# Kernel tuning notes

Hardware: AMD Instinct MI355X
Metric: run time of the kernel (lower is better)

## Reference

```python
import jax, jax.numpy as jnp
import numpy as np

N = 100000
E = 6400000
H = 64  # hidden_nf


def setup_inputs() -> dict:
    key = jax.random.key(0)
    ks = jax.random.split(key, 12)
    x = jax.random.normal(ks[0], (N, 3), dtype=jnp.float32)
    vel = jax.random.normal(ks[1], (N, 3), dtype=jnp.float32)
    vel_norm = jax.random.uniform(ks[2], (N, 1), dtype=jnp.float32)
    edge_index = jax.random.randint(ks[3], (2, E), 0, N, dtype=jnp.int32)
    # coord_mlp_vel: Linear(1,H) -> LeakyReLU(0.2) -> Linear(H,1)
    W1 = jax.random.normal(ks[4], (H, 1), dtype=jnp.float32) * (1.0 / np.sqrt(1))
    b1 = jnp.zeros((H,), dtype=jnp.float32)
    W2 = jax.random.normal(ks[5], (1, H), dtype=jnp.float32) * (1.0 / np.sqrt(H))
    b2 = jnp.zeros((1,), dtype=jnp.float32)
    # phi: Linear(1,H) -> LeakyReLU(0.2) -> Linear(H,1,bias=False, xavier gain=0.001) -> Tanh
    Wp1 = jax.random.normal(ks[6], (H, 1), dtype=jnp.float32) * (1.0 / np.sqrt(1))
    bp1 = jnp.zeros((H,), dtype=jnp.float32)
    Wp2 = jax.random.normal(ks[7], (1, H), dtype=jnp.float32) * 0.001
    return {"x": x, "vel_norm": vel_norm, "vel": vel, "edge_index": edge_index,
            "W1": W1, "b1": b1, "W2": W2, "b2": b2,
            "Wp1": Wp1, "bp1": bp1, "Wp2": Wp2}


def reference(x, vel_norm, vel, edge_index, W1, b1, W2, b2, Wp1, bp1, Wp2):
    row, col = edge_index[0], edge_index[1]
    # edge_model: gather endpoint positions, radial distance -> tiny MLP -> scaled diff
    x_diff = x[row] - x[col]                                   # [E, 3]
    radial = jnp.sqrt(jnp.sum(x_diff * x_diff, axis=1, keepdims=True))  # [E, 1]
    h = jax.nn.leaky_relu(radial @ Wp1.T + bp1, 0.2)           # [E, H]
    e_out = jnp.tanh(h @ Wp2.T)                                # [E, 1]
    m_ij = x_diff * e_out                                      # [E, 3]
    # node_model: unsorted_segment_mean over row
    agg_sum = jax.ops.segment_sum(m_ij, row, num_segments=x.shape[0])           # [N, 3]
    cnt = jax.ops.segment_sum(jnp.ones((m_ij.shape[0], 1), m_ij.dtype), row,
                              num_segments=x.shape[0])                           # [N, 1]
    x_out = x + agg_sum / jnp.maximum(cnt, 1.0)
    # velocity term: x + vel * coord_mlp_vel(vel_norm)
    hv = jax.nn.leaky_relu(vel_norm @ W1.T + b1, 0.2)          # [N, H]
    scale = hv @ W2.T + b2                                     # [N, 1]
    return x_out + vel * scale
```

## Files before the change

### kernel.cpp

```cpp
#include <hip/hip_runtime.h>
#include <hip/hip_fp16.h>
#include <math.h>

#define LEAKY 0.2f
#define HDIM 64
#define EPB 2048
#define TPB1 256
#define PERT (EPB / TPB1)
#define RANGE 1024
#define RSH 10
#define KMAX 128
#define NSLICE 12
#define FIXS 4194304.0f
#define INVFIXS (1.0f / 4194304.0f)


__global__ void precompute_kernel(const float* __restrict__ Wp1,
                                  const float* __restrict__ bp1,
                                  const float* __restrict__ Wp2,
                                  float* __restrict__ consts) {
    int k = threadIdx.x;
    float w1 = Wp1[k];
    float slope = (w1 >= 0.f) ? 1.f : LEAKY;
    float c = Wp2[k] * w1 * slope;
    float bnz = (bp1[k] != 0.f) ? 1.f : 0.f;
    #pragma unroll
    for (int off = 32; off > 0; off >>= 1) {
        c += __shfl_down(c, off, 64);
        bnz += __shfl_down(bnz, off, 64);
    }
    if (k == 0) { consts[0] = c; consts[1] = bnz; }
}

__device__ __forceinline__ float fast_tanh(float v) {
    float e = __builtin_amdgcn_exp2f(v * 2.88539008178f);
    return 1.0f - 2.0f * __builtin_amdgcn_rcpf(e + 1.0f);
}

__device__ __forceinline__ float edge_eo(float rad, float C, bool slow,
                                         const float* sW1, const float* sb1,
                                         const float* sW2) {
    if (!slow) return fast_tanh(C * rad);
    float a = 0.f;
    #pragma unroll
    for (int k = 0; k < HDIM; k++) {
        float h = fmaf(rad, sW1[k], sb1[k]);
        h = (h > 0.f) ? h : LEAKY * h;
        a = fmaf(sW2[k], h, a);
    }
    return fast_tanh(a);
}

__global__ void repack_kernel(const float* __restrict__ x, float4* __restrict__ x4, int N) {
    int i = blockIdx.x * blockDim.x + threadIdx.x;
    if (i < N) x4[i] = make_float4(x[3*i], x[3*i+1], x[3*i+2], 0.f);
}

__global__ void repack_h_kernel(const float* __restrict__ x, uint2* __restrict__ xh, int N) {
    int i = blockIdx.x * blockDim.x + threadIdx.x;
    if (i < N) {
        unsigned hx = __half_as_ushort(__float2half(x[3*i]));
        unsigned hy = __half_as_ushort(__float2half(x[3*i+1]));
        unsigned hz = __half_as_ushort(__float2half(x[3*i+2]));
        xh[i] = make_uint2((hy << 16) | hx, hz);
    }
}

__device__ __forceinline__ unsigned long long pack_rec(float dx, float dy, float dz,
                                                       float eo, unsigned lid) {
    unsigned hx = __half_as_ushort(__float2half(dx * eo));
    unsigned hy = __half_as_ushort(__float2half(dy * eo));
    unsigned hz = __half_as_ushort(__float2half(dz * eo));
    return (unsigned long long)lid
         | ((unsigned long long)hx << 11)
         | ((unsigned long long)hy << 27)
         | ((unsigned long long)hz << 43);
}

__device__ __forceinline__ uint2 make_record(uint2 ga, uint2 gb, int r,
                                             float C, bool slow,
                                             const float* sW1, const float* sb1,
                                             const float* sW2) {
    float ax = __half2float(__ushort_as_half((unsigned short)(ga.x & 0xFFFF)));
    float ay = __half2float(__ushort_as_half((unsigned short)(ga.x >> 16)));
    float az = __half2float(__ushort_as_half((unsigned short)(ga.y & 0xFFFF)));
    float bx = __half2float(__ushort_as_half((unsigned short)(gb.x & 0xFFFF)));
    float by = __half2float(__ushort_as_half((unsigned short)(gb.x >> 16)));
    float bz = __half2float(__ushort_as_half((unsigned short)(gb.y & 0xFFFF)));
    float dx = ax - bx, dy = ay - by, dz = az - bz;
    float rad = sqrtf(dx*dx + dy*dy + dz*dz);
    float eo = edge_eo(rad, C, slow, sW1, sb1, sW2);
    unsigned long long u = pack_rec(dx, dy, dz, eo, (unsigned)r & (RANGE - 1));
    return make_uint2((unsigned)u, (unsigned)(u >> 32));
}

__global__ __launch_bounds__(TPB1) void compute_kernel(
        const uint2* __restrict__ xh,
        const int* __restrict__ ei,
        const float* __restrict__ Wp1, const float* __restrict__ bp1,
        const float* __restrict__ Wp2, const float* __restrict__ consts,
        uint2* __restrict__ rec_raw, unsigned* __restrict__ histG, int E, int K) {
    __shared__ unsigned hist[4][KMAX];
    __shared__ float sW1[HDIM], sb1[HDIM], sW2[HDIM];
    const float C = consts[0];
    const bool slow = (consts[1] != 0.f);
    if (slow) {
        for (int k = threadIdx.x; k < HDIM; k += TPB1) {
            sW1[k] = Wp1[k]; sb1[k] = bp1[k]; sW2[k] = Wp2[k];
        }
    }
    int w = threadIdx.x >> 6;
    for (int k = threadIdx.x; k < 4 * KMAX; k += TPB1) ((unsigned*)hist)[k] = 0;
    __syncthreads();

    const size_t base = (size_t)blockIdx.x * EPB;
    const unsigned t = threadIdx.x;
    if (base + EPB <= (size_t)E && (E & 3) == 0) {
        const int4* pr = (const int4*)(ei + base);
        const int4* pc = (const int4*)(ei + (size_t)E + base);
        int4* po = (int4*)(rec_raw + base);
        const int HALFI4 = EPB / 4;
        #pragma unroll
        for (int i = 0; i < PERT / 4; i++) {
            unsigned idx = t + i * TPB1;
            int4 rv = pr[idx];
            int4 cv = pc[idx];
            uint2 ga0 = xh[rv.x], gb0 = xh[cv.x];
            uint2 ga1 = xh[rv.y], gb1 = xh[cv.y];
            uint2 ga2 = xh[rv.z], gb2 = xh[cv.z];
            uint2 ga3 = xh[rv.w], gb3 = xh[cv.w];
            uint2 r0 = make_record(ga0, gb0, rv.x, C, slow, sW1, sb1, sW2);
            uint2 r1 = make_record(ga1, gb1, rv.y, C, slow, sW1, sb1, sW2);
            uint2 r2 = make_record(ga2, gb2, rv.z, C, slow, sW1, sb1, sW2);
            uint2 r3 = make_record(ga3, gb3, rv.w, C, slow, sW1, sb1, sW2);
            atomicAdd(&hist[w][((unsigned)rv.x) >> RSH], 1u);
            atomicAdd(&hist[w][((unsigned)rv.y) >> RSH], 1u);
            atomicAdd(&hist[w][((unsigned)rv.z) >> RSH], 1u);
            atomicAdd(&hist[w][((unsigned)rv.w) >> RSH], 1u);
            po[idx]          = make_int4((int)r0.x, (int)r0.y, (int)r1.x, (int)r1.y);
            po[HALFI4 + idx] = make_int4((int)r2.x, (int)r2.y, (int)r3.x, (int)r3.y);
        }
    } else {
        for (int i = 0; i < PERT; i++) {
            size_t e = base + (size_t)i * TPB1 + t;
            if (e < (size_t)E) {
                int r = ei[e];
                int c = ei[(size_t)E + e];
                uint2 ga = xh[r], gb = xh[c];
                uint2 rec = make_record(ga, gb, r, C, slow, sW1, sb1, sW2);
                rec_raw[e] = rec;
                atomicAdd(&hist[w][((unsigned)r) >> RSH], 1u);
            }
        }
    }
    __syncthreads();
    for (int k = threadIdx.x; k < K; k += TPB1)
        histG[(size_t)blockIdx.x * K + k] = hist[0][k] + hist[1][k] + hist[2][k] + hist[3][k];
}

__global__ __launch_bounds__(256) void colscan_kernel(unsigned* __restrict__ histG,
                                                      unsigned* __restrict__ totals,
                                                      int nblk, int K) {
    __shared__ unsigned pa[256], pb[256];
    const int b = blockIdx.x;
    const int t = threadIdx.x;
    const int chunk = (nblk + 255) / 256;
    const int r0 = t * chunk;
    unsigned s = 0;
    for (int i = 0; i < chunk; i++) {
        int r = r0 + i;
        if (r < nblk) s += histG[(size_t)r * K + b];
    }
    pa[t] = s;
    __syncthreads();
    unsigned* src = pa; unsigned* dst = pb;
    for (int off = 1; off < 256; off <<= 1) {
        unsigned v = src[t];
        if (t >= off) v += src[t - off];
        dst[t] = v;
        __syncthreads();
        unsigned* tmp = src; src = dst; dst = tmp;
    }
    unsigned excl = (t > 0) ? src[t - 1] : 0u;
    if (t == 255) totals[b] = src[255];
    unsigned run = excl;
    for (int i = 0; i < chunk; i++) {
        int r = r0 + i;
        if (r < nblk) {
            size_t a = (size_t)r * K + b;
            unsigned v = histG[a];
            histG[a] = run;
            run += v;
        }
    }
}

__global__ void base_scan_kernel(const unsigned* __restrict__ totals,
                                 unsigned* __restrict__ base, int K) {
    if (threadIdx.x == 0) {
        unsigned acc = 0;
        for (int k = 0; k < K; k++) { base[k] = acc; acc += totals[k]; }
        base[K] = acc;
    }
}

__global__ __launch_bounds__(TPB1) void sort_kernel(
        const int* __restrict__ ei, const uint2* __restrict__ rec_raw,
        const unsigned* __restrict__ histG, const unsigned* __restrict__ basep,
        uint2* __restrict__ recs, int E, int K) {
    __shared__ uint2 stage[EPB];
    __shared__ unsigned char bucket_of[EPB];
    __shared__ unsigned hist[KMAX];
    __shared__ unsigned scanv[KMAX + 1];
    __shared__ unsigned gstart[KMAX];
    for (int k = threadIdx.x; k < K; k += TPB1) hist[k] = 0;
    __syncthreads();

    const size_t base = (size_t)blockIdx.x * EPB;
    const bool perm = (base + EPB <= (size_t)E) && ((E & 3) == 0);
    uint2 rc[PERT];
    unsigned bk[PERT];
    #pragma unroll
    for (int i = 0; i < PERT; i++) {
        size_t e = base + (size_t)i * TPB1 + threadIdx.x;
        bk[i] = 0xFFFFFFFFu;
        if (e < (size_t)E) {
            size_t pos = e;
            if (perm) {
                unsigned j = (unsigned)(e - base);
                pos = base + ((size_t)((j >> 1) & 1u) * (EPB / 2))
                           + ((j >> 2) << 1) + (j & 1u);
            }
            rc[i] = rec_raw[pos];
            unsigned b_ = ((unsigned)ei[e]) >> RSH;
            bk[i] = b_;
            atomicAdd(&hist[b_], 1u);
        }
    }
    __syncthreads();
    if (threadIdx.x == 0) {
        unsigned a = 0;
        for (int k = 0; k < K; k++) { scanv[k] = a; a += hist[k]; }
        scanv[K] = a;
    }
    __syncthreads();
    if (threadIdx.x < (unsigned)K)
        gstart[threadIdx.x] = basep[threadIdx.x]
                            + histG[(size_t)blockIdx.x * K + threadIdx.x];
    for (int k = threadIdx.x; k < K; k += TPB1) hist[k] = scanv[k];
    __syncthreads();
    #pragma unroll
    for (int i = 0; i < PERT; i++) {
        if (bk[i] != 0xFFFFFFFFu) {
            unsigned slot = atomicAdd(&hist[bk[i]], 1u);
            stage[slot] = rc[i];
            bucket_of[slot] = (unsigned char)bk[i];
        }
    }
    __syncthreads();
    unsigned total = scanv[K];
    for (unsigned j = threadIdx.x; j < total; j += TPB1) {
        unsigned b_ = bucket_of[j];
        recs[(size_t)gstart[b_] + (j - scanv[b_])] = stage[j];
    }
}

__global__ __launch_bounds__(TPB1) void count_kernel(const int* __restrict__ ei,
                                                     unsigned* __restrict__ cnts,
                                                     int E, int K) {
    __shared__ unsigned hist[4][KMAX];
    int w = threadIdx.x >> 6;
    for (int k = threadIdx.x; k < 4 * KMAX; k += TPB1) ((unsigned*)hist)[k] = 0;
    __syncthreads();
    int base = blockIdx.x * EPB;
    #pragma unroll
    for (int i = 0; i < PERT; i++) {
        int e = base + i * TPB1 + threadIdx.x;
        if (e < E) atomicAdd(&hist[w][((unsigned)ei[e]) >> RSH], 1u);
    }
    __syncthreads();
    for (int k = threadIdx.x; k < K; k += TPB1) {
        unsigned t = hist[0][k] + hist[1][k] + hist[2][k] + hist[3][k];
        if (t) atomicAdd(&cnts[k], t);
    }
}

__global__ void scan_kernel(const unsigned* __restrict__ cnts,
                            unsigned* __restrict__ base,
                            unsigned* __restrict__ cursor, int K) {
    if (threadIdx.x == 0) {
        unsigned acc = 0;
        for (int k = 0; k < K; k++) { base[k] = acc; cursor[k] = acc; acc += cnts[k]; }
        base[K] = acc;
    }
}

__global__ __launch_bounds__(TPB1) void bin_kernel(
        const float* __restrict__ x, const float4* __restrict__ x4, int use4,
        const int* __restrict__ ei,
        const float* __restrict__ Wp1, const float* __restrict__ bp1,
        const float* __restrict__ Wp2, const float* __restrict__ consts,
        unsigned* __restrict__ cursor, uint2* __restrict__ recs, int E, int K) {
    __shared__ uint2 stage[EPB];
    __shared__ unsigned char bucket_of[EPB];
    __shared__ unsigned hist[KMAX];
    __shared__ unsigned scanv[KMAX + 1];
    __shared__ unsigned gstart[KMAX];
    __shared__ float sW1[HDIM], sb1[HDIM], sW2[HDIM];
    const float C = consts[0];
    const bool slow = (consts[1] != 0.f);
    if (slow) {
        for (int k = threadIdx.x; k < HDIM; k += TPB1) {
            sW1[k] = Wp1[k]; sb1[k] = bp1[k]; sW2[k] = Wp2[k];
        }
    }
    for (int k = threadIdx.x; k < K; k += TPB1) hist[k] = 0;
    __syncthreads();

    int base = blockIdx.x * EPB;
    uint2 rc[PERT];
    unsigned bk[PERT];
    #pragma unroll
    for (int i = 0; i < PERT; i++) {
        int e = base + i * TPB1 + threadIdx.x;
        bk[i] = 0xFFFFFFFFu;
        if (e < E) {
            int r = ei[e];
            int c = ei[(size_t)E + e];
            float dx, dy, dz;
            if (use4) {
                float4 a = x4[r], b = x4[c];
                dx = a.x - b.x; dy = a.y - b.y; dz = a.z - b.z;
            } else {
                dx = x[3*r]   - x[3*c];
                dy = x[3*r+1] - x[3*c+1];
                dz = x[3*r+2] - x[3*c+2];
            }
            float rad = sqrtf(dx*dx + dy*dy + dz*dz);
            float eo = edge_eo(rad, C, slow, sW1, sb1, sW2);
            unsigned long long u = pack_rec(dx, dy, dz, eo, (unsigned)r & (RANGE - 1));
            rc[i] = make_uint2((unsigned)u, (unsigned)(u >> 32));
            bk[i] = (unsigned)r >> RSH;
            atomicAdd(&hist[bk[i]], 1u);
        }
    }
    __syncthreads();
    if (threadIdx.x == 0) {
        unsigned a = 0;
        for (int k = 0; k < K; k++) { scanv[k] = a; a += hist[k]; }
        scanv[K] = a;
    }
    __syncthreads();
    if (threadIdx.x < (unsigned)K) {
        unsigned c_ = scanv[threadIdx.x + 1] - scanv[threadIdx.x];
        gstart[threadIdx.x] = c_ ? atomicAdd(&cursor[threadIdx.x], c_) : 0u;
    }
    for (int k = threadIdx.x; k < K; k += TPB1) hist[k] = scanv[k];
    __syncthreads();
    #pragma unroll
    for (int i = 0; i < PERT; i++) {
        if (bk[i] != 0xFFFFFFFFu) {
            unsigned slot = atomicAdd(&hist[bk[i]], 1u);
            stage[slot] = rc[i];
            bucket_of[slot] = (unsigned char)bk[i];
        }
    }
    __syncthreads();
    unsigned total = scanv[K];
    for (unsigned j = threadIdx.x; j < total; j += TPB1) {
        unsigned b_ = bucket_of[j];
        recs[(size_t)gstart[b_] + (j - scanv[b_])] = stage[j];
    }
}

__device__ __forceinline__ void proc_rec(uint2 r, unsigned (*acc)[RANGE]) {
    unsigned long long u = ((unsigned long long)r.y << 32) | r.x;
    unsigned lid = (unsigned)(u & (RANGE - 1));
    float mx = __half2float(__ushort_as_half((unsigned short)((u >> 11) & 0xFFFF)));
    float my = __half2float(__ushort_as_half((unsigned short)((u >> 27) & 0xFFFF)));
    float mz = __half2float(__ushort_as_half((unsigned short)((u >> 43) & 0xFFFF)));
    atomicAdd(&acc[0][lid], (unsigned)(int)__float2int_rn(mx * FIXS));
    atomicAdd(&acc[1][lid], (unsigned)(int)__float2int_rn(my * FIXS));
    atomicAdd(&acc[2][lid], (unsigned)(int)__float2int_rn(mz * FIXS));
    atomicAdd(&acc[3][lid], 1u);
}

__global__ __launch_bounds__(256) void reduce_kernel(
        const uint2* __restrict__ recs, const unsigned* __restrict__ base,
        float4* __restrict__ slices, int N, int K) {
    __shared__ unsigned acc[4][RANGE];
    int b = blockIdx.x / NSLICE;
    int s = blockIdx.x % NSLICE;
    for (int i = threadIdx.x; i < RANGE; i += 256) {
        acc[0][i] = 0u; acc[1][i] = 0u; acc[2][i] = 0u; acc[3][i] = 0u;
    }
    __syncthreads();
    unsigned lo = base[b], hi = base[b + 1];
    unsigned cnt = hi - lo;
    unsigned per = (cnt + NSLICE - 1) / NSLICE;
    unsigned st = lo + (unsigned)s * per;
    unsigned en = st + per; if (en > hi) en = hi;
    unsigned j = st + threadIdx.x;
    if (st < hi) {
        while (j + 256 < en) {
            uint2 r0 = recs[j];
            uint2 r1 = recs[j + 256];
            proc_rec(r0, acc);
            proc_rec(r1, acc);
            j += 512;
        }
        while (j < en) { proc_rec(recs[j], acc); j += 256; }
    }
    __syncthreads();
    int nbase = b * RANGE;
    for (int i = threadIdx.x; i < RANGE; i += 256) {
        int node = nbase + i;
        if (node < N)
            slices[(size_t)s * N + node] =
                make_float4((float)(int)acc[0][i] * INVFIXS,
                            (float)(int)acc[1][i] * INVFIXS,
                            (float)(int)acc[2][i] * INVFIXS,
                            (float)acc[3][i]);
    }
}

__global__ void node_kernel(const float* __restrict__ x, const float* __restrict__ vel_norm,
                            const float* __restrict__ vel,
                            const float* __restrict__ W1, const float* __restrict__ b1,
                            const float* __restrict__ W2, const float* __restrict__ b2,
                            const float4* __restrict__ slices,
                            float* __restrict__ out, int N, int S) {
    __shared__ float sW1[HDIM], sb1[HDIM], sW2[HDIM];
    for (int k = threadIdx.x; k < HDIM; k += blockDim.x) {
        sW1[k] = W1[k]; sb1[k] = b1[k]; sW2[k] = W2[k];
    }
    __syncthreads();
    int i = blockIdx.x * blockDim.x + threadIdx.x;
    if (i >= N) return;
    float sx = 0.f, sy = 0.f, sz = 0.f, sc = 0.f;
    for (int s = 0; s < S; s++) {
        float4 v = slices[(size_t)s * N + i];
        sx += v.x; sy += v.y; sz += v.z; sc += v.w;
    }
    float vn = vel_norm[i];
    float a = b2[0];
    #pragma unroll
    for (int k = 0; k < HDIM; k++) {
        float h = fmaf(vn, sW1[k], sb1[k]);
        h = (h > 0.f) ? h : LEAKY * h;
        a = fmaf(sW2[k], h, a);
    }
    float inv = 1.0f / fmaxf(sc, 1.0f);
    out[3*i]     = x[3*i]     + sx * inv + vel[3*i]     * a;
    out[3*i + 1] = x[3*i + 1] + sy * inv + vel[3*i + 1] * a;
    out[3*i + 2] = x[3*i + 2] + sz * inv + vel[3*i + 2] * a;
}

__global__ void edge_atomic_kernel(const float* __restrict__ x, const int* __restrict__ ei,
                                   const float* __restrict__ Wp1, const float* __restrict__ bp1,
                                   const float* __restrict__ Wp2, const float* __restrict__ consts,
                                   float* __restrict__ acc, int E) {
    __shared__ float sW1[HDIM], sb1[HDIM], sW2[HDIM];
    const float C = consts[0];
    const bool slow = (consts[1] != 0.f);
    if (slow) {
        for (int k = threadIdx.x; k < HDIM; k += blockDim.x) {
            sW1[k] = Wp1[k]; sb1[k] = bp1[k]; sW2[k] = Wp2[k];
        }
        __syncthreads();
    }
    int e = blockIdx.x * blockDim.x + threadIdx.x;
    if (e >= E) return;
    int r = ei[e];
    int c = ei[E + e];
    float dx = x[3*r] - x[3*c];
    float dy = x[3*r+1] - x[3*c+1];
    float dz = x[3*r+2] - x[3*c+2];
    float rad = sqrtf(dx*dx + dy*dy + dz*dz);
    float eo = edge_eo(rad, C, slow, sW1, sb1, sW2);
    float* basep = acc + ((size_t)r << 2);
    atomicAdd(basep + 0, dx * eo);
    atomicAdd(basep + 1, dy * eo);
    atomicAdd(basep + 2, dz * eo);
    atomicAdd(basep + 3, 1.f);
}

extern "C" void kernel_launch(void* const* d_in, const int* in_sizes, int n_in,
                              void* d_out, int out_size, void* d_ws, size_t ws_size,
                              hipStream_t stream) {
    const float* x        = (const float*)d_in[0];
    const float* vel_norm = (const float*)d_in[1];
    const float* vel      = (const float*)d_in[2];
    const int*   ei       = (const int*)  d_in[3];
    const float* W1       = (const float*)d_in[4];
    const float* b1       = (const float*)d_in[5];
    const float* W2       = (const float*)d_in[6];
    const float* b2       = (const float*)d_in[7];
    const float* Wp1      = (const float*)d_in[8];
    const float* bp1      = (const float*)d_in[9];
    const float* Wp2      = (const float*)d_in[10];

    const int N = in_sizes[0] / 3;
    const int E = in_sizes[3] / 2;
    const int K = (N + RANGE - 1) / RANGE;
    const int nblk = (E + EPB - 1) / EPB;

    size_t rec_bytes   = (size_t)E * sizeof(uint2);
    size_t slice_bytes = (size_t)NSLICE * N * sizeof(float4);
    size_t x4_bytes    = (size_t)N * sizeof(float4);
    size_t histG_bytes = (size_t)nblk * K * sizeof(unsigned);

    size_t sp_raw   = rec_bytes;
    size_t sp_x4    = sp_raw + (rec_bytes > slice_bytes ? rec_bytes : slice_bytes);
    size_t sp_hist  = sp_x4 + x4_bytes;
    size_t sp_tot   = sp_hist + histG_bytes;
    size_t sp_base  = sp_tot + (size_t)K * sizeof(unsigned);
    size_t sp_const = (sp_base + (size_t)(K + 1) * sizeof(unsigned) + 15) & ~(size_t)15;
    size_t need_split = sp_const + 32;

    size_t small_bytes = (size_t)(KMAX + (KMAX + 1) + KMAX) * sizeof(unsigned) + 32;
    size_t fu_recs  = slice_bytes;
    size_t fu_x4    = fu_recs + rec_bytes;
    size_t fu_small = fu_x4 + x4_bytes;
    size_t need_fused = fu_small + small_bytes;

    if (K <= KMAX && ws_size >= need_split) {
        uint2*    recs   = (uint2*)   d_ws;
        uint2*    raw    = (uint2*)   ((char*)d_ws + sp_raw);
        float4*   slices = (float4*)  ((char*)d_ws + sp_raw);
        uint2*    xh     = (uint2*)   ((char*)d_ws + sp_x4);
        unsigned* histG  = (unsigned*)((char*)d_ws + sp_hist);
        unsigned* totals = (unsigned*)((char*)d_ws + sp_tot);
        unsigned* basep  = (unsigned*)((char*)d_ws + sp_base);
        float*    consts = (float*)   ((char*)d_ws + sp_const);

        precompute_kernel<<<1, 64, 0, stream>>>(Wp1, bp1, Wp2, consts);
        repack_h_kernel<<<(N + 255) / 256, 256, 0, stream>>>(x, xh, N);
        compute_kernel<<<nblk, TPB1, 0, stream>>>(xh, ei, Wp1, bp1, Wp2, consts,
                                                  raw, histG, E, K);
        colscan_kernel<<<K, 256, 0, stream>>>(histG, totals, nblk, K);
        base_scan_kernel<<<1, 64, 0, stream>>>(totals, basep, K);
        sort_kernel<<<nblk, TPB1, 0, stream>>>(ei, raw, histG, basep, recs, E, K);
        reduce_kernel<<<K * NSLICE, 256, 0, stream>>>(recs, basep, slices, N, K);
        node_kernel<<<(N + 255) / 256, 256, 0, stream>>>(x, vel_norm, vel, W1, b1, W2, b2,
                                                         slices, (float*)d_out, N, NSLICE);
    } else if (K <= KMAX && ws_size >= need_fused) {
        float4*   slices = (float4*)  d_ws;
        uint2*    recs   = (uint2*)   ((char*)d_ws + fu_recs);
        float4*   x4     = (float4*)  ((char*)d_ws + fu_x4);
        unsigned* cnts   = (unsigned*)((char*)d_ws + fu_small);
        unsigned* basep  = cnts + KMAX;
        unsigned* cursor = basep + KMAX + 1;
        float*    consts = (float*)(cursor + KMAX);

        hipMemsetAsync(cnts, 0, small_bytes, stream);
        precompute_kernel<<<1, 64, 0, stream>>>(Wp1, bp1, Wp2, consts);
        repack_kernel<<<(N + 255) / 256, 256, 0, stream>>>(x, x4, N);
        count_kernel<<<nblk, TPB1, 0, stream>>>(ei, cnts, E, K);
        scan_kernel<<<1, 64, 0, stream>>>(cnts, basep, cursor, K);
        bin_kernel<<<nblk, TPB1, 0, stream>>>(x, x4, 1, ei, Wp1, bp1, Wp2, consts,
                                              cursor, recs, E, K);
        reduce_kernel<<<K * NSLICE, 256, 0, stream>>>(recs, basep, slices, N, K);
        node_kernel<<<(N + 255) / 256, 256, 0, stream>>>(x, vel_norm, vel, W1, b1, W2, b2,
                                                         slices, (float*)d_out, N, NSLICE);
    } else {
        float* acc    = (float*)d_ws;
        float* consts = (float*)((char*)d_ws + (size_t)N * sizeof(float4));
        hipMemsetAsync(d_ws, 0, (size_t)N * sizeof(float4) + 32, stream);
        precompute_kernel<<<1, 64, 0, stream>>>(Wp1, bp1, Wp2, consts);
        edge_atomic_kernel<<<(E + 255) / 256, 256, 0, stream>>>(x, ei, Wp1, bp1, Wp2,
                                                                consts, acc, E);
        node_kernel<<<(N + 255) / 256, 256, 0, stream>>>(x, vel_norm, vel, W1, b1, W2, b2,
                                                         (const float4*)acc, (float*)d_out, N, 1);
    }
}
```

Measured before the change: 223.6 us.

## Fuse edge record computation into sort pass, replace compute with count-only histogram

The first pass now only reads row indices to build per-block bucket histograms, and the sort pass itself gathers endpoint positions, computes the edge records and scatters them. This removes the write and re-read of the intermediate raw record array (8 bytes per edge each way). The cost is that the count pass reads the row indices separately and the sort kernel carries more register pressure from the gather and MLP work. The workspace layout drops the raw buffer aliasing.

```diff
diff --git a/kernel.cpp b/kernel.cpp
--- a/kernel.cpp
+++ b/kernel.cpp
@@ -94,64 +94,27 @@
     return make_uint2((unsigned)u, (unsigned)(u >> 32));
 }
 
-__global__ __launch_bounds__(TPB1) void compute_kernel(
-        const uint2* __restrict__ xh,
-        const int* __restrict__ ei,
-        const float* __restrict__ Wp1, const float* __restrict__ bp1,
-        const float* __restrict__ Wp2, const float* __restrict__ consts,
-        uint2* __restrict__ rec_raw, unsigned* __restrict__ histG, int E, int K) {
+__global__ __launch_bounds__(TPB1) void count2_kernel(const int* __restrict__ ei,
+                                                      unsigned* __restrict__ histG,
+                                                      int E, int K) {
     __shared__ unsigned hist[4][KMAX];
-    __shared__ float sW1[HDIM], sb1[HDIM], sW2[HDIM];
-    const float C = consts[0];
-    const bool slow = (consts[1] != 0.f);
-    if (slow) {
-        for (int k = threadIdx.x; k < HDIM; k += TPB1) {
-            sW1[k] = Wp1[k]; sb1[k] = bp1[k]; sW2[k] = Wp2[k];
-        }
-    }
     int w = threadIdx.x >> 6;
     for (int k = threadIdx.x; k < 4 * KMAX; k += TPB1) ((unsigned*)hist)[k] = 0;
     __syncthreads();
-
     const size_t base = (size_t)blockIdx.x * EPB;
-    const unsigned t = threadIdx.x;
-    if (base + EPB <= (size_t)E && (E & 3) == 0) {
-        const int4* pr = (const int4*)(ei + base);
-        const int4* pc = (const int4*)(ei + (size_t)E + base);
-        int4* po = (int4*)(rec_raw + base);
-        const int HALFI4 = EPB / 4;
+    if (base + EPB <= (size_t)E) {
+        const int4* p = (const int4*)(ei + base);
         #pragma unroll
-        for (int i = 0; i < PERT / 4; i++) {
-            unsigned idx = t + i * TPB1;
-            int4 rv = pr[idx];
-            int4 cv = pc[idx];
-            uint2 ga0 = xh[rv.x], gb0 = xh[cv.x];
-            uint2 ga1 = xh[rv.y], gb1 = xh[cv.y];
-            uint2 ga2 = xh[rv.z], gb2 = xh[cv.z];
-            uint2 ga3 = xh[rv.w], gb3 = xh[cv.w];
-            uint2 r0 = make_record(ga0, gb0, rv.x, C, slow, sW1, sb1, sW2);
-            uint2 r1 = make_record(ga1, gb1, rv.y, C, slow, sW1, sb1, sW2);
-            uint2 r2 = make_record(ga2, gb2, rv.z, C, slow, sW1, sb1, sW2);
-            uint2 r3 = make_record(ga3, gb3, rv.w, C, slow, sW1, sb1, sW2);
-            atomicAdd(&hist[w][((unsigned)rv.x) >> RSH], 1u);
-            atomicAdd(&hist[w][((unsigned)rv.y) >> RSH], 1u);
-            atomicAdd(&hist[w][((unsigned)rv.z) >> RSH], 1u);
-            atomicAdd(&hist[w][((unsigned)rv.w) >> RSH], 1u);
-            po[idx]          = make_int4((int)r0.x, (int)r0.y, (int)r1.x, (int)r1.y);
-            po[HALFI4 + idx] = make_int4((int)r2.x, (int)r2.y, (int)r3.x, (int)r3.y);
+        for (int i = 0; i < EPB / 4 / TPB1; i++) {
+            int4 v = p[threadIdx.x + i * TPB1];
+            atomicAdd(&hist[w][((unsigned)v.x) >> RSH], 1u);
+            atomicAdd(&hist[w][((unsigned)v.y) >> RSH], 1u);
+            atomicAdd(&hist[w][((unsigned)v.z) >> RSH], 1u);
+            atomicAdd(&hist[w][((unsigned)v.w) >> RSH], 1u);
         }
     } else {
-        for (int i = 0; i < PERT; i++) {
-            size_t e = base + (size_t)i * TPB1 + t;
-            if (e < (size_t)E) {
-                int r = ei[e];
-                int c = ei[(size_t)E + e];
-                uint2 ga = xh[r], gb = xh[c];
-                uint2 rec = make_record(ga, gb, r, C, slow, sW1, sb1, sW2);
-                rec_raw[e] = rec;
-                atomicAdd(&hist[w][((unsigned)r) >> RSH], 1u);
-            }
-        }
+        for (size_t e = base + threadIdx.x; e < (size_t)E; e += TPB1)
+            atomicAdd(&hist[w][((unsigned)ei[e]) >> RSH], 1u);
     }
     __syncthreads();
     for (int k = threadIdx.x; k < K; k += TPB1)
@@ -204,8 +167,11 @@
     }
 }
 
-__global__ __launch_bounds__(TPB1) void sort_kernel(
-        const int* __restrict__ ei, const uint2* __restrict__ rec_raw,
+__global__ __launch_bounds__(TPB1) void fused_kernel(
+        const uint2* __restrict__ xh,
+        const int* __restrict__ ei,
+        const float* __restrict__ Wp1, const float* __restrict__ bp1,
+        const float* __restrict__ Wp2, const float* __restrict__ consts,
         const unsigned* __restrict__ histG, const unsigned* __restrict__ basep,
         uint2* __restrict__ recs, int E, int K) {
     __shared__ uint2 stage[EPB];
@@ -213,41 +179,71 @@
     __shared__ unsigned hist[KMAX];
     __shared__ unsigned scanv[KMAX + 1];
     __shared__ unsigned gstart[KMAX];
+    __shared__ float sW1[HDIM], sb1[HDIM], sW2[HDIM];
+    const float C = consts[0];
+    const bool slow = (consts[1] != 0.f);
+    if (slow) {
+        for (int k = threadIdx.x; k < HDIM; k += TPB1) {
+            sW1[k] = Wp1[k]; sb1[k] = bp1[k]; sW2[k] = Wp2[k];
+        }
+    }
     for (int k = threadIdx.x; k < K; k += TPB1) hist[k] = 0;
     __syncthreads();
 
     const size_t base = (size_t)blockIdx.x * EPB;
-    const bool perm = (base + EPB <= (size_t)E) && ((E & 3) == 0);
+    const unsigned t = threadIdx.x;
     uint2 rc[PERT];
     unsigned bk[PERT];
-    #pragma unroll
-    for (int i = 0; i < PERT; i++) {
-        size_t e = base + (size_t)i * TPB1 + threadIdx.x;
-        bk[i] = 0xFFFFFFFFu;
-        if (e < (size_t)E) {
-            size_t pos = e;
-            if (perm) {
-                unsigned j = (unsigned)(e - base);
-                pos = base + ((size_t)((j >> 1) & 1u) * (EPB / 2))
-                           + ((j >> 2) << 1) + (j & 1u);
+    if (base + EPB <= (size_t)E && (E & 3) == 0) {
+        const int4* pr = (const int4*)(ei + base);
+        const int4* pc = (const int4*)(ei + (size_t)E + base);
+        #pragma unroll
+        for (int i = 0; i < PERT / 4; i++) {
+            unsigned idx = t + i * TPB1;
+            int4 rv = pr[idx];
+            int4 cv = pc[idx];
+            uint2 ga0 = xh[rv.x], gb0 = xh[cv.x];
+            uint2 ga1 = xh[rv.y], gb1 = xh[cv.y];
+            uint2 ga2 = xh[rv.z], gb2 = xh[cv.z];
+            uint2 ga3 = xh[rv.w], gb3 = xh[cv.w];
+            rc[i*4 + 0] = make_record(ga0, gb0, rv.x, C, slow, sW1, sb1, sW2);
+            rc[i*4 + 1] = make_record(ga1, gb1, rv.y, C, slow, sW1, sb1, sW2);
+            rc[i*4 + 2] = make_record(ga2, gb2, rv.z, C, slow, sW1, sb1, sW2);
+            rc[i*4 + 3] = make_record(ga3, gb3, rv.w, C, slow, sW1, sb1, sW2);
+            bk[i*4 + 0] = (unsigned)rv.x >> RSH;
+            bk[i*4 + 1] = (unsigned)rv.y >> RSH;
+            bk[i*4 + 2] = (unsigned)rv.z >> RSH;
+            bk[i*4 + 3] = (unsigned)rv.w >> RSH;
+            atomicAdd(&hist[bk[i*4 + 0]], 1u);
+            atomicAdd(&hist[bk[i*4 + 1]], 1u);
+            atomicAdd(&hist[bk[i*4 + 2]], 1u);
+            atomicAdd(&hist[bk[i*4 + 3]], 1u);
+        }
+    } else {
+        #pragma unroll
+        for (int i = 0; i < PERT; i++) {
+            size_t e = base + (size_t)i * TPB1 + t;
+            bk[i] = 0xFFFFFFFFu;
+            if (e < (size_t)E) {
+                int r = ei[e];
+                int c = ei[(size_t)E + e];
+                uint2 ga = xh[r], gb = xh[c];
+                rc[i] = make_record(ga, gb, r, C, slow, sW1, sb1, sW2);
+                bk[i] = (unsigned)r >> RSH;
+                atomicAdd(&hist[bk[i]], 1u);
             }
-            rc[i] = rec_raw[pos];
-            unsigned b_ = ((unsigned)ei[e]) >> RSH;
-            bk[i] = b_;
-            atomicAdd(&hist[b_], 1u);
-        }
-    }
-    __syncthreads();
-    if (threadIdx.x == 0) {
+        }
+    }
+    __syncthreads();
+    if (t == 0) {
         unsigned a = 0;
         for (int k = 0; k < K; k++) { scanv[k] = a; a += hist[k]; }
         scanv[K] = a;
     }
     __syncthreads();
-    if (threadIdx.x < (unsigned)K)
-        gstart[threadIdx.x] = basep[threadIdx.x]
-                            + histG[(size_t)blockIdx.x * K + threadIdx.x];
-    for (int k = threadIdx.x; k < K; k += TPB1) hist[k] = scanv[k];
+    if (t < (unsigned)K)
+        gstart[t] = basep[t] + histG[(size_t)blockIdx.x * K + t];
+    for (int k = t; k < K; k += TPB1) hist[k] = scanv[k];
     __syncthreads();
     #pragma unroll
     for (int i = 0; i < PERT; i++) {
@@ -259,7 +255,7 @@
     }
     __syncthreads();
     unsigned total = scanv[K];
-    for (unsigned j = threadIdx.x; j < total; j += TPB1) {
+    for (unsigned j = t; j < total; j += TPB1) {
         unsigned b_ = bucket_of[j];
         recs[(size_t)gstart[b_] + (j - scanv[b_])] = stage[j];
     }
@@ -510,12 +506,12 @@
     size_t x4_bytes    = (size_t)N * sizeof(float4);
     size_t histG_bytes = (size_t)nblk * K * sizeof(unsigned);
 
-    size_t sp_raw   = rec_bytes;
-    size_t sp_x4    = sp_raw + (rec_bytes > slice_bytes ? rec_bytes : slice_bytes);
-    size_t sp_hist  = sp_x4 + x4_bytes;
-    size_t sp_tot   = sp_hist + histG_bytes;
-    size_t sp_base  = sp_tot + (size_t)K * sizeof(unsigned);
-    size_t sp_const = (sp_base + (size_t)(K + 1) * sizeof(unsigned) + 15) & ~(size_t)15;
+    size_t sp_slices = rec_bytes;
+    size_t sp_xh     = sp_slices + slice_bytes;
+    size_t sp_hist   = sp_xh + x4_bytes;
+    size_t sp_tot    = sp_hist + histG_bytes;
+    size_t sp_base   = sp_tot + (size_t)K * sizeof(unsigned);
+    size_t sp_const  = (sp_base + (size_t)(K + 1) * sizeof(unsigned) + 15) & ~(size_t)15;
     size_t need_split = sp_const + 32;
 
     size_t small_bytes = (size_t)(KMAX + (KMAX + 1) + KMAX) * sizeof(unsigned) + 32;
@@ -526,9 +522,8 @@
 
     if (K <= KMAX && ws_size >= need_split) {
         uint2*    recs   = (uint2*)   d_ws;
-        uint2*    raw    = (uint2*)   ((char*)d_ws + sp_raw);
-        float4*   slices = (float4*)  ((char*)d_ws + sp_raw);
-        uint2*    xh     = (uint2*)   ((char*)d_ws + sp_x4);
+        float4*   slices = (float4*)  ((char*)d_ws + sp_slices);
+        uint2*    xh     = (uint2*)   ((char*)d_ws + sp_xh);
         unsigned* histG  = (unsigned*)((char*)d_ws + sp_hist);
         unsigned* totals = (unsigned*)((char*)d_ws + sp_tot);
         unsigned* basep  = (unsigned*)((char*)d_ws + sp_base);
@@ -536,11 +531,11 @@
 
         precompute_kernel<<<1, 64, 0, stream>>>(Wp1, bp1, Wp2, consts);
         repack_h_kernel<<<(N + 255) / 256, 256, 0, stream>>>(x, xh, N);
-        compute_kernel<<<nblk, TPB1, 0, stream>>>(xh, ei, Wp1, bp1, Wp2, consts,
-                                                  raw, histG, E, K);
+        count2_kernel<<<nblk, TPB1, 0, stream>>>(ei, histG, E, K);
         colscan_kernel<<<K, 256, 0, stream>>>(histG, totals, nblk, K);
         base_scan_kernel<<<1, 64, 0, stream>>>(totals, basep, K);
-        sort_kernel<<<nblk, TPB1, 0, stream>>>(ei, raw, histG, basep, recs, E, K);
+        fused_kernel<<<nblk, TPB1, 0, stream>>>(xh, ei, Wp1, bp1, Wp2, consts,
+                                                histG, basep, recs, E, K);
         reduce_kernel<<<K * NSLICE, 256, 0, stream>>>(recs, basep, slices, N, K);
         node_kernel<<<(N + 255) / 256, 256, 0, stream>>>(x, vel_norm, vel, W1, b1, W2, b2,
                                                          slices, (float*)d_out, N, NSLICE);
```

New measurement: 210.2 us. -6.0%, faster.
